# Performance work log

Hardware: AMD Instinct MI355X
Metric: run time of the kernel (lower is better)

The kernel has to match this reference:

```python
import jax, jax.numpy as jnp
import numpy as np

T, N, E = 12, 100000, 3200000
F = H = 64
O, L = 32, 2


def setup_inputs() -> dict:
    key = jax.random.key(0)
    ks = jax.random.split(key, 13)
    sc = 0.08  # keep gate pre-activations in a sane range
    return {
        "x": jax.random.normal(ks[0], (T, N, F), jnp.float32),
        "hidden_states": jax.random.normal(ks[1], (L, N, H), jnp.float32),
        "cell_states": jax.random.normal(ks[2], (L, N, H), jnp.float32),
        "Wx_self": jax.random.normal(ks[3], (L, 4, F, H), jnp.float32) * sc,
        "Wx_neigh": jax.random.normal(ks[4], (L, 4, F, H), jnp.float32) * sc,
        "Wh_self": jax.random.normal(ks[5], (L, 4, H, H), jnp.float32) * sc,
        "Wh_neigh": jax.random.normal(ks[6], (L, 4, H, H), jnp.float32) * sc,
        "w_c": jax.random.normal(ks[7], (L, 3, H), jnp.float32) * sc,  # peephole i,f,o
        "bias": jax.random.normal(ks[8], (L, 4, H), jnp.float32) * sc,  # i,f,c,o
        "Wout": jax.random.normal(ks[9], (H, O), jnp.float32) * sc,
        "bout": jax.random.normal(ks[10], (O,), jnp.float32) * sc,
        "src": jax.random.randint(ks[11], (E,), 0, N, jnp.int32),
        "dst": jax.random.randint(ks[12], (E,), 0, N, jnp.int32),
    }


def reference(x, hidden_states, cell_states, Wx_self, Wx_neigh, Wh_self,
              Wh_neigh, w_c, bias, Wout, bout, src, dst):
    # mean aggregation over incoming edges (DGL copy_u + mean reduce)
    deg = jax.ops.segment_sum(jnp.ones((E,), x.dtype), dst, num_segments=N)
    deg_inv = jnp.where(deg > 0, 1.0 / deg, 0.0)[:, None]  # [N,1]

    def mean_agg(feat):  # [N,D] -> [N,D]
        return jax.ops.segment_sum(feat[src], dst, num_segments=N) * deg_inv

    def gates(feat, agg, Ws, Wn):  # Ws,Wn: [4,D,H] -> [4,N,H]
        return (jnp.einsum('nf,gfh->gnh', feat, Ws)
                + jnp.einsum('nf,gfh->gnh', agg, Wn))

    def step(carry, x_t):
        hs, cs = carry  # [L,N,H] each
        inp = x_t
        new_h, new_c = [], []
        for j in range(L):
            h, c = hs[j], cs[j]
            x_agg = mean_agg(inp)  # reuse_msg_passing: one agg shared by 4 gates
            h_agg = mean_agg(h)
            pre = gates(inp, x_agg, Wx_self[j], Wx_neigh[j]) \
                + gates(h, h_agg, Wh_self[j], Wh_neigh[j])  # [4,N,H]
            i = jax.nn.sigmoid(pre[0] + w_c[j, 0] * c + bias[j, 0])
            f = jax.nn.sigmoid(pre[1] + w_c[j, 1] * c + bias[j, 1])
            c_tilde = jnp.tanh(pre[2] + bias[j, 2])
            nc = f * c + i * c_tilde
            o = jax.nn.sigmoid(pre[3] + w_c[j, 2] * nc + bias[j, 3])
            nh = o * jnp.tanh(nc)
            new_h.append(nh)
            new_c.append(nc)
            inp = nh
        out_t = inp @ Wout + bout  # [N,O]
        return (jnp.stack(new_h), jnp.stack(new_c)), out_t

    (h_f, c_f), outs = jax.lax.scan(step, (hidden_states, cell_states), x)
    return outs, h_f, c_f  # outs: [T,N,O]
```

## Files before the change

kernel.cpp:

```cpp
#include <hip/hip_runtime.h>

#define T_STEPS 12
#define NN 100000
#define EE 3200000
#define HD 64
#define OD 32
#define NBK 391

typedef __attribute__((ext_vector_type(8))) short short8;
typedef __attribute__((ext_vector_type(4))) float f32x4;
typedef __attribute__((ext_vector_type(2))) float f32x2;
typedef unsigned short u16;
typedef unsigned char u8;

__device__ __forceinline__ u16 f2b(float x) {
  union { float f; unsigned u; } v; v.f = x;
  unsigned r = v.u + 0x7FFFu + ((v.u >> 16) & 1u);
  return (u16)(r >> 16);
}
__device__ __forceinline__ u16 f2h(float x) {
  union { _Float16 h; u16 s; } u; u.h = (_Float16)x; return u.s;
}
__device__ __forceinline__ float h2f(u16 s) {
  union { u16 s; _Float16 h; } u; u.s = s; return (float)u.h;
}
__device__ __forceinline__ float sigm(float x) {
  x = fminf(fmaxf(x, -30.f), 30.f);
  return 1.0f / (1.0f + __expf(-x));
}
__device__ __forceinline__ float tanh_f(float x) {
  x = fminf(fmaxf(x, -15.f), 15.f);
  float e = __expf(2.0f * x);
  return (e - 1.0f) / (e + 1.0f);
}

__device__ __forceinline__ uint2 pack8_fp8(const float* f) {
  unsigned lo = 0, hi = 0;
  lo = __builtin_amdgcn_cvt_pk_fp8_f32(f[0], f[1], lo, false);
  lo = __builtin_amdgcn_cvt_pk_fp8_f32(f[2], f[3], lo, true);
  hi = __builtin_amdgcn_cvt_pk_fp8_f32(f[4], f[5], hi, false);
  hi = __builtin_amdgcn_cvt_pk_fp8_f32(f[6], f[7], hi, true);
  return make_uint2(lo, hi);
}
__device__ __forceinline__ u8 f2q(float x) {
  return (u8)(__builtin_amdgcn_cvt_pk_fp8_f32(x, 0.f, 0u, false) & 0xFFu);
}
__device__ __forceinline__ void acc8_fp8(uint2 v, float* a) {
  f32x2 p0 = __builtin_amdgcn_cvt_pk_f32_fp8(v.x, false);
  f32x2 p1 = __builtin_amdgcn_cvt_pk_f32_fp8(v.x, true);
  f32x2 p2 = __builtin_amdgcn_cvt_pk_f32_fp8(v.y, false);
  f32x2 p3 = __builtin_amdgcn_cvt_pk_f32_fp8(v.y, true);
  a[0] += p0[0]; a[1] += p0[1]; a[2] += p1[0]; a[3] += p1[1];
  a[4] += p2[0]; a[5] += p2[1]; a[6] += p3[0]; a[7] += p3[1];
}
__device__ __forceinline__ void dec16_acc2(uint4 q, f32x2* a) {
  a[0] += __builtin_amdgcn_cvt_pk_f32_fp8(q.x, false);
  a[1] += __builtin_amdgcn_cvt_pk_f32_fp8(q.x, true);
  a[2] += __builtin_amdgcn_cvt_pk_f32_fp8(q.y, false);
  a[3] += __builtin_amdgcn_cvt_pk_f32_fp8(q.y, true);
  a[4] += __builtin_amdgcn_cvt_pk_f32_fp8(q.z, false);
  a[5] += __builtin_amdgcn_cvt_pk_f32_fp8(q.z, true);
  a[6] += __builtin_amdgcn_cvt_pk_f32_fp8(q.w, false);
  a[7] += __builtin_amdgcn_cvt_pk_f32_fp8(q.w, true);
}
__device__ __forceinline__ short8 s8_from_fp8(uint2 q) {
  f32x2 p0 = __builtin_amdgcn_cvt_pk_f32_fp8(q.x, false);
  f32x2 p1 = __builtin_amdgcn_cvt_pk_f32_fp8(q.x, true);
  f32x2 p2 = __builtin_amdgcn_cvt_pk_f32_fp8(q.y, false);
  f32x2 p3 = __builtin_amdgcn_cvt_pk_f32_fp8(q.y, true);
  short8 o;
  o[0] = (short)f2b(p0[0]); o[1] = (short)f2b(p0[1]);
  o[2] = (short)f2b(p1[0]); o[3] = (short)f2b(p1[1]);
  o[4] = (short)f2b(p2[0]); o[5] = (short)f2b(p2[1]);
  o[6] = (short)f2b(p3[0]); o[7] = (short)f2b(p3[1]);
  return o;
}
__device__ __forceinline__ short8 s8_from_f32(float4 a, float4 b) {
  short8 o;
  o[0] = (short)f2b(a.x); o[1] = (short)f2b(a.y);
  o[2] = (short)f2b(a.z); o[3] = (short)f2b(a.w);
  o[4] = (short)f2b(b.x); o[5] = (short)f2b(b.y);
  o[6] = (short)f2b(b.z); o[7] = (short)f2b(b.w);
  return o;
}

__global__ __launch_bounds__(256) void k_bhist(const int* __restrict__ dst,
                                               int* __restrict__ bcnt, int E) {
  __shared__ int h[NBK];
  for (int i = threadIdx.x; i < NBK; i += 256) h[i] = 0;
  __syncthreads();
  int base = blockIdx.x * 4096;
#pragma unroll
  for (int i = 0; i < 16; ++i) {
    int e = base + i * 256 + threadIdx.x;
    if (e < E) atomicAdd(&h[dst[e] >> 8], 1);
  }
  __syncthreads();
  for (int i = threadIdx.x; i < NBK; i += 256)
    if (h[i]) atomicAdd(&bcnt[i], h[i]);
}

__global__ __launch_bounds__(512) void k_bscan(const int* __restrict__ bcnt,
                                               int* __restrict__ bbase,
                                               int* __restrict__ bcur) {
  __shared__ int buf[512];
  int tid = threadIdx.x;
  int v = (tid < NBK) ? bcnt[tid] : 0;
  buf[tid] = v;
  __syncthreads();
  for (int off = 1; off < 512; off <<= 1) {
    int t = (tid >= off) ? buf[tid - off] : 0;
    __syncthreads();
    buf[tid] += t;
    __syncthreads();
  }
  if (tid < NBK) {
    int e = buf[tid] - v;
    bbase[tid] = e;
    bcur[tid] = e;
  }
}

__global__ __launch_bounds__(256) void k_bscatter(const int* __restrict__ src,
                                                  const int* __restrict__ dst,
                                                  int* __restrict__ bcur,
                                                  uint2* __restrict__ binned, int E) {
  __shared__ int h[NBK];
  __shared__ int base[NBK];
  __shared__ int cur[NBK];
  for (int i = threadIdx.x; i < NBK; i += 256) { h[i] = 0; cur[i] = 0; }
  __syncthreads();
  int b0 = blockIdx.x * 4096;
  int d[16], s[16];
#pragma unroll
  for (int i = 0; i < 16; ++i) {
    int e = b0 + i * 256 + threadIdx.x;
    if (e < E) {
      d[i] = dst[e];
      s[i] = src[e];
      atomicAdd(&h[d[i] >> 8], 1);
    } else d[i] = -1;
  }
  __syncthreads();
  for (int i = threadIdx.x; i < NBK; i += 256)
    if (h[i]) base[i] = atomicAdd(&bcur[i], h[i]);
  __syncthreads();
#pragma unroll
  for (int i = 0; i < 16; ++i) {
    if (d[i] >= 0) {
      int bk = d[i] >> 8;
      int r = atomicAdd(&cur[bk], 1);
      binned[base[bk] + r] = make_uint2((unsigned)s[i], (unsigned)d[i]);
    }
  }
}

__global__ __launch_bounds__(256) void k_bsort(const uint2* __restrict__ binned,
                                               const int* __restrict__ bbase,
                                               const int* __restrict__ bcnt,
                                               int* __restrict__ csr,
                                               int* __restrict__ row_ptr,
                                               float* __restrict__ deg_inv, int n) {
  __shared__ int cnt[256];
  __shared__ int buf[256];
  __shared__ int cur[256];
  int b = blockIdx.x, tid = threadIdx.x;
  int ebase = bbase[b];
  int ecnt = bcnt[b];
  cnt[tid] = 0;
  __syncthreads();
  for (int i = tid; i < ecnt; i += 256)
    atomicAdd(&cnt[binned[ebase + i].y & 255], 1);
  __syncthreads();
  int v = cnt[tid];
  buf[tid] = v;
  __syncthreads();
  for (int off = 1; off < 256; off <<= 1) {
    int t = (tid >= off) ? buf[tid - off] : 0;
    __syncthreads();
    buf[tid] += t;
    __syncthreads();
  }
  int excl = buf[tid] - v;
  int node = b * 256 + tid;
  if (node < n) {
    row_ptr[node] = ebase + excl;
    deg_inv[node] = v ? (1.0f / (float)v) : 0.0f;
  }
  if (b == NBK - 1 && tid == 0) row_ptr[n] = ebase + ecnt;
  cur[tid] = excl;
  __syncthreads();
  for (int i = tid; i < ecnt; i += 256) {
    uint2 pr = binned[ebase + i];
    int pos = atomicAdd(&cur[pr.y & 255], 1);
    csr[ebase + pos] = (int)pr.x;
  }
}

__global__ __launch_bounds__(256) void k_prep(const float* __restrict__ Wxs,
                                              const float* __restrict__ Wxn,
                                              const float* __restrict__ Whs,
                                              const float* __restrict__ Whn,
                                              u16* __restrict__ bprep) {
  int idx = blockIdx.x * 256 + threadIdx.x;
  int l = idx >> 16;
  int kb = (idx >> 13) & 7;
  int fi = (idx >> 9) & 15;
  int ln = (idx >> 3) & 63;
  int j = idx & 7;
  int fc = kb * 32 + ((ln >> 4) << 3) + j;
  int g = fi & 3;
  int kk = ((fi >> 2) << 4) + (ln & 15);
  int t = fc >> 6, f = fc & 63;
  const float* tabs[4] = {Wxs, Wxn, Whs, Whn};
  bprep[idx] = f2b(tabs[t][((size_t)(l * 4 + g) * 64 + f) * 64 + kk]);
}

__global__ __launch_bounds__(256) void k_prepw(const float* __restrict__ Wout,
                                               u16* __restrict__ wp) {
  int idx = blockIdx.x * 256 + threadIdx.x;
  int kb = idx >> 10;
  int fi = (idx >> 9) & 1;
  int ln = (idx >> 3) & 63;
  int j = idx & 7;
  int k = kb * 32 + ((ln >> 4) << 3) + j;
  int o = fi * 16 + (ln & 15);
  wp[idx] = f2b(Wout[k * 32 + o]);
}

__global__ __launch_bounds__(256) void k_convxall(const float* __restrict__ x,
                                                  u8* __restrict__ XQ) {
  int tid = blockIdx.x * 256 + threadIdx.x;
  int j = tid & 7;
  int tn = tid >> 3;
  int n = tn % NN;
  int t = tn / NN;
  const float* rp = x + (size_t)tn * 64 + j * 8;
  float4 v0 = *reinterpret_cast<const float4*>(rp);
  float4 v1 = *reinterpret_cast<const float4*>(rp + 4);
  float f[8] = {v0.x, v0.y, v0.z, v0.w, v1.x, v1.y, v1.z, v1.w};
  *reinterpret_cast<uint2*>(XQ + (size_t)n * 768 + t * 64 + j * 8) = pack8_fp8(f);
}

__global__ __launch_bounds__(256) void k_inith(const float* __restrict__ h0,
                                               const float* __restrict__ c0,
                                               u16* __restrict__ H0bf,
                                               u16* __restrict__ L1bf,
                                               u8* __restrict__ HQ,
                                               u16* __restrict__ C16) {
  int idx = blockIdx.x * 256 + threadIdx.x;
  int n = idx >> 3, j = idx & 7;
#pragma unroll
  for (int L = 0; L < 2; ++L) {
    const float* rp = h0 + (size_t)L * NN * 64 + (size_t)n * 64 + j * 8;
    float4 v0 = *reinterpret_cast<const float4*>(rp);
    float4 v1 = *reinterpret_cast<const float4*>(rp + 4);
    float f[8] = {v0.x, v0.y, v0.z, v0.w, v1.x, v1.y, v1.z, v1.w};
    short8 o;
#pragma unroll
    for (int i = 0; i < 8; ++i) o[i] = (short)f2b(f[i]);
    if (L == 0)
      *reinterpret_cast<short8*>(H0bf + (size_t)n * 64 + j * 8) = o;
    else
      *reinterpret_cast<short8*>(L1bf + (size_t)n * 64 + j * 8) = o;
    *reinterpret_cast<uint2*>(HQ + (size_t)n * 128 + L * 64 + j * 8) = pack8_fp8(f);
    const float* cp = c0 + (size_t)L * NN * 64 + (size_t)n * 64 + j * 8;
    float4 c0v = *reinterpret_cast<const float4*>(cp);
    float4 c1v = *reinterpret_cast<const float4*>(cp + 4);
    float cf[8] = {c0v.x, c0v.y, c0v.z, c0v.w, c1v.x, c1v.y, c1v.z, c1v.w};
    short8 oc;
#pragma unroll
    for (int i = 0; i < 8; ++i) oc[i] = (short)f2h(cf[i]);
    *reinterpret_cast<short8*>(C16 + (size_t)L * NN * 64 + (size_t)n * 64 + j * 8) = oc;
  }
}

__global__ __launch_bounds__(256) void k_aggx(const u8* __restrict__ XQ,
                                              const int* __restrict__ row_ptr,
                                              const int* __restrict__ csr,
                                              const float* __restrict__ deg_inv,
                                              u8* __restrict__ AGGXq) {
  int node = blockIdx.x * 4 + (threadIdx.x >> 6);
  int p = blockIdx.y;
  int lane = threadIdx.x & 63;
  int g = lane >> 4, m = lane & 15;
  int start = row_ptr[node], end = row_ptr[node + 1];
  const size_t poff = (size_t)p * 256 + m * 16;
  f32x2 a[8];
#pragma unroll
  for (int i = 0; i < 8; ++i) a[i] = (f32x2){0.f, 0.f};
  int e = start + g;
  for (; e + 12 < end; e += 16) {
    int s0 = csr[e], s1 = csr[e + 4], s2 = csr[e + 8], s3 = csr[e + 12];
    uint4 q0 = *reinterpret_cast<const uint4*>(XQ + (size_t)s0 * 768 + poff);
    uint4 q1 = *reinterpret_cast<const uint4*>(XQ + (size_t)s1 * 768 + poff);
    uint4 q2 = *reinterpret_cast<const uint4*>(XQ + (size_t)s2 * 768 + poff);
    uint4 q3 = *reinterpret_cast<const uint4*>(XQ + (size_t)s3 * 768 + poff);
    dec16_acc2(q0, a); dec16_acc2(q1, a); dec16_acc2(q2, a); dec16_acc2(q3, a);
  }
  if (e + 4 < end) {
    int s0 = csr[e], s1 = csr[e + 4];
    uint4 q0 = *reinterpret_cast<const uint4*>(XQ + (size_t)s0 * 768 + poff);
    uint4 q1 = *reinterpret_cast<const uint4*>(XQ + (size_t)s1 * 768 + poff);
    dec16_acc2(q0, a); dec16_acc2(q1, a);
    e += 8;
  }
  if (e < end) {
    int s0 = csr[e];
    uint4 q0 = *reinterpret_cast<const uint4*>(XQ + (size_t)s0 * 768 + poff);
    dec16_acc2(q0, a);
  }
#pragma unroll
  for (int off = 16; off < 64; off <<= 1)
#pragma unroll
    for (int i = 0; i < 8; ++i) {
      a[i][0] += __shfl_xor(a[i][0], off);
      a[i][1] += __shfl_xor(a[i][1], off);
    }
  if (g == 0) {
    float sc = deg_inv[node];
    float f[16];
#pragma unroll
    for (int i = 0; i < 8; ++i) {
      f[i * 2] = a[i][0] * sc;
      f[i * 2 + 1] = a[i][1] * sc;
    }
    uint4 o;
    unsigned w;
    w = 0; w = __builtin_amdgcn_cvt_pk_fp8_f32(f[0], f[1], w, false);
    w = __builtin_amdgcn_cvt_pk_fp8_f32(f[2], f[3], w, true); o.x = w;
    w = 0; w = __builtin_amdgcn_cvt_pk_fp8_f32(f[4], f[5], w, false);
    w = __builtin_amdgcn_cvt_pk_fp8_f32(f[6], f[7], w, true); o.y = w;
    w = 0; w = __builtin_amdgcn_cvt_pk_fp8_f32(f[8], f[9], w, false);
    w = __builtin_amdgcn_cvt_pk_fp8_f32(f[10], f[11], w, true); o.z = w;
    w = 0; w = __builtin_amdgcn_cvt_pk_fp8_f32(f[12], f[13], w, false);
    w = __builtin_amdgcn_cvt_pk_fp8_f32(f[14], f[15], w, true); o.w = w;
    int t = p * 4 + (m >> 2);
    *reinterpret_cast<uint4*>(AGGXq + ((size_t)t * NN + node) * 64 + (m & 3) * 16) = o;
  }
}

__global__ __launch_bounds__(256) void k_agg_pair(const u8* __restrict__ Q,
                                                  const int* __restrict__ row_ptr,
                                                  const int* __restrict__ csr,
                                                  const float* __restrict__ deg_inv,
                                                  u16* __restrict__ out0,
                                                  u16* __restrict__ out1) {
  int node = blockIdx.x * 4 + (threadIdx.x >> 6);
  int lane = threadIdx.x & 63;
  int g = lane >> 4, m = lane & 15;
  int start = row_ptr[node], end = row_ptr[node + 1];
  float a[8] = {0, 0, 0, 0, 0, 0, 0, 0};
  int e = start + g;
  for (; e + 12 < end; e += 16) {
    int s0 = csr[e], s1 = csr[e + 4], s2 = csr[e + 8], s3 = csr[e + 12];
    uint2 v0 = *reinterpret_cast<const uint2*>(Q + (size_t)s0 * 128 + m * 8);
    uint2 v1 = *reinterpret_cast<const uint2*>(Q + (size_t)s1 * 128 + m * 8);
    uint2 v2 = *reinterpret_cast<const uint2*>(Q + (size_t)s2 * 128 + m * 8);
    uint2 v3 = *reinterpret_cast<const uint2*>(Q + (size_t)s3 * 128 + m * 8);
    acc8_fp8(v0, a); acc8_fp8(v1, a); acc8_fp8(v2, a); acc8_fp8(v3, a);
  }
  if (e + 4 < end) {
    int s0 = csr[e], s1 = csr[e + 4];
    uint2 v0 = *reinterpret_cast<const uint2*>(Q + (size_t)s0 * 128 + m * 8);
    uint2 v1 = *reinterpret_cast<const uint2*>(Q + (size_t)s1 * 128 + m * 8);
    acc8_fp8(v0, a); acc8_fp8(v1, a);
    e += 8;
  }
  if (e < end) {
    int s0 = csr[e];
    uint2 v0 = *reinterpret_cast<const uint2*>(Q + (size_t)s0 * 128 + m * 8);
    acc8_fp8(v0, a);
  }
#pragma unroll
  for (int off = 16; off < 64; off <<= 1) {
#pragma unroll
    for (int i = 0; i < 8; ++i) a[i] += __shfl_xor(a[i], off);
  }
  if (g == 0) {
    float sc = deg_inv[node];
    short8 o;
#pragma unroll
    for (int i = 0; i < 8; ++i) o[i] = (short)f2b(a[i] * sc);
    if (m < 8)
      *reinterpret_cast<short8*>(out0 + (size_t)node * 64 + m * 8) = o;
    else
      *reinterpret_cast<short8*>(out1 + (size_t)node * 64 + (m - 8) * 8) = o;
  }
}

__global__ __launch_bounds__(256, 2) void k_gates0(
    const float* __restrict__ xin, const u8* __restrict__ aggxq,
    u16* __restrict__ h0bf, const u16* __restrict__ aggh0,
    u8* __restrict__ hq, u16* __restrict__ c16,
    float* __restrict__ hf32, float* __restrict__ cf32,
    const u16* __restrict__ bprepl,
    const float* __restrict__ wcl, const float* __restrict__ biasl,
    int n_nodes, int wf) {
  const int tid = threadIdx.x;
  const int lane = tid & 63;
  const int w = tid >> 6;
  const int nb = blockIdx.x * 64;
  const int cl = lane & 15;
  const int kg = lane >> 4;

  short8 breg[8][4];
#pragma unroll
  for (int kb = 0; kb < 8; ++kb)
#pragma unroll
    for (int fl = 0; fl < 4; ++fl)
      breg[kb][fl] = *reinterpret_cast<const short8*>(
          bprepl + (kb << 13) + (((w << 2) + fl) << 9) + (lane << 3));

  int gnc[4];
#pragma unroll
  for (int rg = 0; rg < 4; ++rg) {
    int g = nb + rg * 16 + cl;
    gnc[rg] = (g < n_nodes) ? g : (n_nodes - 1);
  }

  f32x4 acc[4][4];
  f32x4 z4 = {0.f, 0.f, 0.f, 0.f};
#pragma unroll
  for (int a = 0; a < 4; ++a)
#pragma unroll
    for (int b = 0; b < 4; ++b) acc[a][b] = z4;

  const int koff = kg << 3;
#pragma unroll
  for (int kb = 0; kb < 8; ++kb) {
    const int idx = ((kb & 1) << 5) + koff;
#pragma unroll
    for (int rg = 0; rg < 4; ++rg) {
      short8 a;
      if (kb < 2) {
        const float* rp = xin + (size_t)gnc[rg] * 64 + idx;
        a = s8_from_f32(*reinterpret_cast<const float4*>(rp),
                        *reinterpret_cast<const float4*>(rp + 4));
      } else if (kb < 4) {
        a = s8_from_fp8(*reinterpret_cast<const uint2*>(aggxq + (size_t)gnc[rg] * 64 + idx));
      } else if (kb < 6) {
        a = *reinterpret_cast<const short8*>(h0bf + (size_t)gnc[rg] * 64 + idx);
      } else {
        a = *reinterpret_cast<const short8*>(aggh0 + (size_t)gnc[rg] * 64 + idx);
      }
      acc[rg][0] = __builtin_amdgcn_mfma_f32_16x16x32_bf16(a, breg[kb][0], acc[rg][0], 0, 0, 0);
      acc[rg][1] = __builtin_amdgcn_mfma_f32_16x16x32_bf16(a, breg[kb][1], acc[rg][1], 0, 0, 0);
      acc[rg][2] = __builtin_amdgcn_mfma_f32_16x16x32_bf16(a, breg[kb][2], acc[rg][2], 0, 0, 0);
      acc[rg][3] = __builtin_amdgcn_mfma_f32_16x16x32_bf16(a, breg[kb][3], acc[rg][3], 0, 0, 0);
    }
  }
  __syncthreads();

  const int k = (w << 4) + cl;
  const float wci = wcl[k], wcf = wcl[64 + k], wco = wcl[128 + k];
  const float bi = biasl[k], bfg = biasl[64 + k], bc = biasl[128 + k], bo = biasl[192 + k];
#pragma unroll
  for (int rg = 0; rg < 4; ++rg) {
#pragma unroll
    for (int r = 0; r < 4; ++r) {
      int n = nb + rg * 16 + kg * 4 + r;
      if (n < n_nodes) {
        size_t off = (size_t)n * 64 + k;
        float c_old = h2f(c16[off]);
        float ig = sigm(acc[rg][0][r] + wci * c_old + bi);
        float fg = sigm(acc[rg][1][r] + wcf * c_old + bfg);
        float ct = tanh_f(acc[rg][2][r] + bc);
        float nc = fg * c_old + ig * ct;
        float og = sigm(acc[rg][3][r] + wco * nc + bo);
        float nh = og * tanh_f(nc);
        c16[off] = f2h(nc);
        h0bf[off] = f2b(nh);
        hq[(size_t)n * 128 + k] = f2q(nh);
        if (wf) { hf32[off] = nh; cf32[off] = nc; }
      }
    }
  }
}

__global__ __launch_bounds__(256, 2) void k_gates1(
    const u16* __restrict__ h0bf, const u16* __restrict__ aggh0,
    const u16* __restrict__ aggh1,
    u16* __restrict__ l1bf, u8* __restrict__ hq, u16* __restrict__ c16,
    float* __restrict__ hf32, float* __restrict__ cf32,
    const u16* __restrict__ bprepl,
    const float* __restrict__ wcl, const float* __restrict__ biasl,
    const u16* __restrict__ wproj, const float* __restrict__ boutp,
    float* __restrict__ outp, int n_nodes, int wf) {
  __shared__ u16 Hsm[64 * 64];
  const int tid = threadIdx.x;
  const int lane = tid & 63;
  const int w = tid >> 6;
  const int nb = blockIdx.x * 64;
  const int cl = lane & 15;
  const int kg = lane >> 4;

  short8 breg[8][4];
#pragma unroll
  for (int kb = 0; kb < 8; ++kb)
#pragma unroll
    for (int fl = 0; fl < 4; ++fl)
      breg[kb][fl] = *reinterpret_cast<const short8*>(
          bprepl + (kb << 13) + (((w << 2) + fl) << 9) + (lane << 3));

  int gnc[4];
#pragma unroll
  for (int rg = 0; rg < 4; ++rg) {
    int g = nb + rg * 16 + cl;
    gnc[rg] = (g < n_nodes) ? g : (n_nodes - 1);
  }

  f32x4 acc[4][4];
  f32x4 z4 = {0.f, 0.f, 0.f, 0.f};
#pragma unroll
  for (int a = 0; a < 4; ++a)
#pragma unroll
    for (int b = 0; b < 4; ++b) acc[a][b] = z4;

  const int koff = kg << 3;
#pragma unroll
  for (int kb = 0; kb < 8; ++kb) {
    const int idx = ((kb & 1) << 5) + koff;
#pragma unroll
    for (int rg = 0; rg < 4; ++rg) {
      short8 a;
      if (kb < 2) {
        a = *reinterpret_cast<const short8*>(h0bf + (size_t)gnc[rg] * 64 + idx);
      } else if (kb < 4) {
        a = *reinterpret_cast<const short8*>(aggh0 + (size_t)gnc[rg] * 64 + idx);
      } else if (kb < 6) {
        a = *reinterpret_cast<const short8*>(l1bf + (size_t)gnc[rg] * 64 + idx);
      } else {
        a = *reinterpret_cast<const short8*>(aggh1 + (size_t)gnc[rg] * 64 + idx);
      }
      acc[rg][0] = __builtin_amdgcn_mfma_f32_16x16x32_bf16(a, breg[kb][0], acc[rg][0], 0, 0, 0);
      acc[rg][1] = __builtin_amdgcn_mfma_f32_16x16x32_bf16(a, breg[kb][1], acc[rg][1], 0, 0, 0);
      acc[rg][2] = __builtin_amdgcn_mfma_f32_16x16x32_bf16(a, breg[kb][2], acc[rg][2], 0, 0, 0);
      acc[rg][3] = __builtin_amdgcn_mfma_f32_16x16x32_bf16(a, breg[kb][3], acc[rg][3], 0, 0, 0);
    }
  }
  __syncthreads();

  const int k = (w << 4) + cl;
  const float wci = wcl[k], wcf = wcl[64 + k], wco = wcl[128 + k];
  const float bi = biasl[k], bfg = biasl[64 + k], bc = biasl[128 + k], bo = biasl[192 + k];
#pragma unroll
  for (int rg = 0; rg < 4; ++rg) {
#pragma unroll
    for (int r = 0; r < 4; ++r) {
      int n = nb + rg * 16 + kg * 4 + r;
      if (n < n_nodes) {
        size_t off = (size_t)n * 64 + k;
        float c_old = h2f(c16[off]);
        float ig = sigm(acc[rg][0][r] + wci * c_old + bi);
        float fg = sigm(acc[rg][1][r] + wcf * c_old + bfg);
        float ct = tanh_f(acc[rg][2][r] + bc);
        float nc = fg * c_old + ig * ct;
        float og = sigm(acc[rg][3][r] + wco * nc + bo);
        float nh = og * tanh_f(nc);
        c16[off] = f2h(nc);
        u16 hb = f2b(nh);
        l1bf[off] = hb;
        hq[(size_t)n * 128 + 64 + k] = f2q(nh);
        Hsm[(rg * 16 + kg * 4 + r) * 64 + k] = hb;
        if (wf) { hf32[off] = nh; cf32[off] = nc; }
      }
    }
  }

  __syncthreads();
  short8 bw[2][2];
#pragma unroll
  for (int kb = 0; kb < 2; ++kb)
#pragma unroll
    for (int fi = 0; fi < 2; ++fi)
      bw[kb][fi] = *reinterpret_cast<const short8*>(wproj + (((kb * 2 + fi) * 64 + lane) << 3));
  short8 a0 = *reinterpret_cast<const short8*>(&Hsm[(w * 16 + cl) * 64 + kg * 8]);
  short8 a1 = *reinterpret_cast<const short8*>(&Hsm[(w * 16 + cl) * 64 + 32 + kg * 8]);
  f32x4 p0 = z4, p1 = z4;
  p0 = __builtin_amdgcn_mfma_f32_16x16x32_bf16(a0, bw[0][0], p0, 0, 0, 0);
  p0 = __builtin_amdgcn_mfma_f32_16x16x32_bf16(a1, bw[1][0], p0, 0, 0, 0);
  p1 = __builtin_amdgcn_mfma_f32_16x16x32_bf16(a0, bw[0][1], p1, 0, 0, 0);
  p1 = __builtin_amdgcn_mfma_f32_16x16x32_bf16(a1, bw[1][1], p1, 0, 0, 0);
  const float bo0 = boutp[cl], bo1 = boutp[16 + cl];
#pragma unroll
  for (int r = 0; r < 4; ++r) {
    int n = nb + w * 16 + kg * 4 + r;
    if (n < n_nodes) {
      outp[(size_t)n * OD + cl] = p0[r] + bo0;
      outp[(size_t)n * OD + 16 + cl] = p1[r] + bo1;
    }
  }
}

extern "C" void kernel_launch(void* const* d_in, const int* in_sizes, int n_in,
                              void* d_out, int out_size, void* d_ws, size_t ws_size,
                              hipStream_t stream) {
  const float* x = (const float*)d_in[0];
  const float* h0 = (const float*)d_in[1];
  const float* c0 = (const float*)d_in[2];
  const float* Wxs = (const float*)d_in[3];
  const float* Wxn = (const float*)d_in[4];
  const float* Whs = (const float*)d_in[5];
  const float* Whn = (const float*)d_in[6];
  const float* wc = (const float*)d_in[7];
  const float* bias = (const float*)d_in[8];
  const float* Wout = (const float*)d_in[9];
  const float* bout = (const float*)d_in[10];
  const int* src = (const int*)d_in[11];
  const int* dst = (const int*)d_in[12];

  float* out = (float*)d_out;
  float* outs = out;
  float* hstate = out + (size_t)T_STEPS * NN * OD;
  float* cstate = hstate + (size_t)2 * NN * HD;

  char* p = (char*)d_ws;
  auto alloc = [&](size_t bytes) {
    char* r = p;
    p += (bytes + 255) & ~(size_t)255;
    return r;
  };
  int* csr = (int*)alloc((size_t)EE * 4);
  u8* XQ = (u8*)alloc((size_t)NN * 768);
  uint2* binned = (uint2*)XQ;
  u8* AGGXq = (u8*)alloc((size_t)T_STEPS * NN * 64);
  int* row_ptr = (int*)alloc((size_t)(NN + 1) * 4);
  int* bcnt = (int*)alloc(NBK * 4);
  int* bbase = (int*)alloc(NBK * 4);
  int* bcur = (int*)alloc(NBK * 4);
  float* deg_inv = (float*)alloc((size_t)NN * 4);
  u16* H0bf = (u16*)alloc((size_t)NN * 64 * 2);
  u16* L1bf = (u16*)alloc((size_t)NN * 64 * 2);
  u8* HQ = (u8*)alloc((size_t)NN * 128);
  u16* AGGH0 = (u16*)alloc((size_t)NN * 64 * 2);
  u16* AGGH1 = (u16*)alloc((size_t)NN * 64 * 2);
  u16* C16 = (u16*)alloc((size_t)2 * NN * 64 * 2);
  u16* bprep = (u16*)alloc((size_t)2 * 65536 * 2);
  u16* wprep = (u16*)alloc((size_t)2048 * 2);

  const int nchunk = (EE + 4095) / 4096;

  hipMemsetAsync(bcnt, 0, (size_t)NBK * 4, stream);
  k_bhist<<<nchunk, 256, 0, stream>>>(dst, bcnt, EE);
  k_bscan<<<1, 512, 0, stream>>>(bcnt, bbase, bcur);
  k_bscatter<<<nchunk, 256, 0, stream>>>(src, dst, bcur, binned, EE);
  k_bsort<<<NBK, 256, 0, stream>>>(binned, bbase, bcnt, csr, row_ptr, deg_inv, NN);
  k_prep<<<512, 256, 0, stream>>>(Wxs, Wxn, Whs, Whn, bprep);
  k_prepw<<<8, 256, 0, stream>>>(Wout, wprep);
  k_convxall<<<(T_STEPS * NN * 8 + 255) / 256, 256, 0, stream>>>(x, XQ);
  k_inith<<<NN * 8 / 256, 256, 0, stream>>>(h0, c0, H0bf, L1bf, HQ, C16);
  {
    dim3 g((NN + 3) / 4, 3);
    k_aggx<<<g, 256, 0, stream>>>(XQ, row_ptr, csr, deg_inv, AGGXq);
  }
  k_agg_pair<<<(NN + 3) / 4, 256, 0, stream>>>(HQ, row_ptr, csr, deg_inv, AGGH0, AGGH1);

  for (int t = 0; t < T_STEPS; ++t) {
    int wf = (t == T_STEPS - 1) ? 1 : 0;
    k_gates0<<<(NN + 63) / 64, 256, 0, stream>>>(
        x + (size_t)t * NN * HD, AGGXq + (size_t)t * NN * 64,
        H0bf, AGGH0, HQ, C16, hstate, cstate, bprep, wc, bias, NN, wf);
    k_agg_pair<<<(NN + 3) / 4, 256, 0, stream>>>(HQ, row_ptr, csr, deg_inv, AGGH0, AGGH1);
    k_gates1<<<(NN + 63) / 64, 256, 0, stream>>>(
        H0bf, AGGH0, AGGH1, L1bf, HQ, C16 + (size_t)NN * 64,
        hstate + (size_t)NN * HD, cstate + (size_t)NN * HD,
        bprep + 65536, wc + 192, bias + 256,
        wprep, bout, outs + (size_t)t * NN * OD, NN, wf);
  }
}
```

Measured before the change: 2.887 ms.

## Fuse per-step neighbor aggregation into layer-1 gates kernel with LDS staging

Removes the separate per-step pair aggregation kernel. The layer-1 gate kernel now gathers the fp8 neighbor features for both layers itself, stores them in swizzled shared memory and feeds them straight into the MFMA loop. It also writes AGGH0 out for the next step's layer-0 kernel. The interleaved fp8 hidden table is split into separate layer-0 and layer-1 tables, and layer 1 is double-buffered so in-place updates do not race with neighbor reads from other blocks. This saves a launch and the bf16 aggregate round-trip through global memory. In exchange the gates kernel uses more shared memory and becomes a latency-bound gather, which may lower occupancy.

Result: slower. 3.231 ms (+11.9%).

```diff
diff --git a/kernel.cpp b/kernel.cpp
--- a/kernel.cpp
+++ b/kernel.cpp
@@ -44,14 +44,6 @@
 }
 __device__ __forceinline__ u8 f2q(float x) {
   return (u8)(__builtin_amdgcn_cvt_pk_fp8_f32(x, 0.f, 0u, false) & 0xFFu);
-}
-__device__ __forceinline__ void acc8_fp8(uint2 v, float* a) {
-  f32x2 p0 = __builtin_amdgcn_cvt_pk_f32_fp8(v.x, false);
-  f32x2 p1 = __builtin_amdgcn_cvt_pk_f32_fp8(v.x, true);
-  f32x2 p2 = __builtin_amdgcn_cvt_pk_f32_fp8(v.y, false);
-  f32x2 p3 = __builtin_amdgcn_cvt_pk_f32_fp8(v.y, true);
-  a[0] += p0[0]; a[1] += p0[1]; a[2] += p1[0]; a[3] += p1[1];
-  a[4] += p2[0]; a[5] += p2[1]; a[6] += p3[0]; a[7] += p3[1];
 }
 __device__ __forceinline__ void dec16_acc2(uint4 q, f32x2* a) {
   a[0] += __builtin_amdgcn_cvt_pk_f32_fp8(q.x, false);
@@ -246,7 +238,8 @@
                                                const float* __restrict__ c0,
                                                u16* __restrict__ H0bf,
                                                u16* __restrict__ L1bf,
-                                               u8* __restrict__ HQ,
+                                               u8* __restrict__ HQ0,
+                                               u8* __restrict__ HQ1,
                                                u16* __restrict__ C16) {
   int idx = blockIdx.x * 256 + threadIdx.x;
   int n = idx >> 3, j = idx & 7;
@@ -259,11 +252,13 @@
     short8 o;
 #pragma unroll
     for (int i = 0; i < 8; ++i) o[i] = (short)f2b(f[i]);
-    if (L == 0)
+    if (L == 0) {
       *reinterpret_cast<short8*>(H0bf + (size_t)n * 64 + j * 8) = o;
-    else
+      *reinterpret_cast<uint2*>(HQ0 + (size_t)n * 64 + j * 8) = pack8_fp8(f);
+    } else {
       *reinterpret_cast<short8*>(L1bf + (size_t)n * 64 + j * 8) = o;
-    *reinterpret_cast<uint2*>(HQ + (size_t)n * 128 + L * 64 + j * 8) = pack8_fp8(f);
+      *reinterpret_cast<uint2*>(HQ1 + (size_t)n * 64 + j * 8) = pack8_fp8(f);
+    }
     const float* cp = c0 + (size_t)L * NN * 64 + (size_t)n * 64 + j * 8;
     float4 c0v = *reinterpret_cast<const float4*>(cp);
     float4 c1v = *reinterpret_cast<const float4*>(cp + 4);
@@ -340,59 +335,53 @@
   }
 }
 
-__global__ __launch_bounds__(256) void k_agg_pair(const u8* __restrict__ Q,
-                                                  const int* __restrict__ row_ptr,
-                                                  const int* __restrict__ csr,
-                                                  const float* __restrict__ deg_inv,
-                                                  u16* __restrict__ out0,
-                                                  u16* __restrict__ out1) {
-  int node = blockIdx.x * 4 + (threadIdx.x >> 6);
+__global__ __launch_bounds__(256) void k_agg0(const u8* __restrict__ HQ0,
+                                              const int* __restrict__ row_ptr,
+                                              const int* __restrict__ csr,
+                                              const float* __restrict__ deg_inv,
+                                              u16* __restrict__ aggh0, int n_nodes) {
   int lane = threadIdx.x & 63;
-  int g = lane >> 4, m = lane & 15;
-  int start = row_ptr[node], end = row_ptr[node + 1];
-  float a[8] = {0, 0, 0, 0, 0, 0, 0, 0};
-  int e = start + g;
-  for (; e + 12 < end; e += 16) {
-    int s0 = csr[e], s1 = csr[e + 4], s2 = csr[e + 8], s3 = csr[e + 12];
-    uint2 v0 = *reinterpret_cast<const uint2*>(Q + (size_t)s0 * 128 + m * 8);
-    uint2 v1 = *reinterpret_cast<const uint2*>(Q + (size_t)s1 * 128 + m * 8);
-    uint2 v2 = *reinterpret_cast<const uint2*>(Q + (size_t)s2 * 128 + m * 8);
-    uint2 v3 = *reinterpret_cast<const uint2*>(Q + (size_t)s3 * 128 + m * 8);
-    acc8_fp8(v0, a); acc8_fp8(v1, a); acc8_fp8(v2, a); acc8_fp8(v3, a);
-  }
-  if (e + 4 < end) {
-    int s0 = csr[e], s1 = csr[e + 4];
-    uint2 v0 = *reinterpret_cast<const uint2*>(Q + (size_t)s0 * 128 + m * 8);
-    uint2 v1 = *reinterpret_cast<const uint2*>(Q + (size_t)s1 * 128 + m * 8);
-    acc8_fp8(v0, a); acc8_fp8(v1, a);
-    e += 8;
-  }
-  if (e < end) {
-    int s0 = csr[e];
-    uint2 v0 = *reinterpret_cast<const uint2*>(Q + (size_t)s0 * 128 + m * 8);
-    acc8_fp8(v0, a);
-  }
-#pragma unroll
-  for (int off = 16; off < 64; off <<= 1) {
-#pragma unroll
-    for (int i = 0; i < 8; ++i) a[i] += __shfl_xor(a[i], off);
-  }
-  if (g == 0) {
+  int w = threadIdx.x >> 6;
+  int ng = lane >> 2, m = lane & 3;
+  int node = blockIdx.x * 64 + w * 16 + ng;
+  int nodec = (node < n_nodes) ? node : (n_nodes - 1);
+  int start = row_ptr[nodec], end = row_ptr[nodec + 1];
+  const int coff = m * 16;
+  f32x2 a[8];
+#pragma unroll
+  for (int i = 0; i < 8; ++i) a[i] = (f32x2){0.f, 0.f};
+  int e = start;
+  for (; e + 3 < end; e += 4) {
+    int s0 = csr[e], s1 = csr[e + 1], s2 = csr[e + 2], s3 = csr[e + 3];
+    uint4 q0 = *reinterpret_cast<const uint4*>(HQ0 + (size_t)s0 * 64 + coff);
+    uint4 q1 = *reinterpret_cast<const uint4*>(HQ0 + (size_t)s1 * 64 + coff);
+    uint4 q2 = *reinterpret_cast<const uint4*>(HQ0 + (size_t)s2 * 64 + coff);
+    uint4 q3 = *reinterpret_cast<const uint4*>(HQ0 + (size_t)s3 * 64 + coff);
+    dec16_acc2(q0, a); dec16_acc2(q1, a); dec16_acc2(q2, a); dec16_acc2(q3, a);
+  }
+  for (; e < end; ++e) {
+    uint4 q0 = *reinterpret_cast<const uint4*>(HQ0 + (size_t)csr[e] * 64 + coff);
+    dec16_acc2(q0, a);
+  }
+  if (node < n_nodes) {
     float sc = deg_inv[node];
-    short8 o;
-#pragma unroll
-    for (int i = 0; i < 8; ++i) o[i] = (short)f2b(a[i] * sc);
-    if (m < 8)
-      *reinterpret_cast<short8*>(out0 + (size_t)node * 64 + m * 8) = o;
-    else
-      *reinterpret_cast<short8*>(out1 + (size_t)node * 64 + (m - 8) * 8) = o;
+    short8 o0, o1;
+#pragma unroll
+    for (int i = 0; i < 4; ++i) {
+      o0[i * 2] = (short)f2b(a[i][0] * sc);
+      o0[i * 2 + 1] = (short)f2b(a[i][1] * sc);
+      o1[i * 2] = (short)f2b(a[4 + i][0] * sc);
+      o1[i * 2 + 1] = (short)f2b(a[4 + i][1] * sc);
+    }
+    *reinterpret_cast<short8*>(aggh0 + (size_t)node * 64 + m * 16) = o0;
+    *reinterpret_cast<short8*>(aggh0 + (size_t)node * 64 + m * 16 + 8) = o1;
   }
 }
 
 __global__ __launch_bounds__(256, 2) void k_gates0(
     const float* __restrict__ xin, const u8* __restrict__ aggxq,
     u16* __restrict__ h0bf, const u16* __restrict__ aggh0,
-    u8* __restrict__ hq, u16* __restrict__ c16,
+    u8* __restrict__ hq0, u16* __restrict__ c16,
     float* __restrict__ hf32, float* __restrict__ cf32,
     const u16* __restrict__ bprepl,
     const float* __restrict__ wcl, const float* __restrict__ biasl,
@@ -471,30 +460,84 @@
         float nh = og * tanh_f(nc);
         c16[off] = f2h(nc);
         h0bf[off] = f2b(nh);
-        hq[(size_t)n * 128 + k] = f2q(nh);
+        hq0[off] = f2q(nh);
         if (wf) { hf32[off] = nh; cf32[off] = nc; }
       }
     }
   }
 }
 
-__global__ __launch_bounds__(256, 2) void k_gates1(
-    const u16* __restrict__ h0bf, const u16* __restrict__ aggh0,
-    const u16* __restrict__ aggh1,
-    u16* __restrict__ l1bf, u8* __restrict__ hq, u16* __restrict__ c16,
+__global__ __launch_bounds__(256, 2) void k_pg1(
+    const u8* __restrict__ HQ0, const u8* __restrict__ HQ1r,
+    u8* __restrict__ HQ1w,
+    const int* __restrict__ row_ptr, const int* __restrict__ csr,
+    const float* __restrict__ deg_inv,
+    u16* __restrict__ aggh0,
+    const u16* __restrict__ h0bf, u16* __restrict__ l1bf, u16* __restrict__ c16,
     float* __restrict__ hf32, float* __restrict__ cf32,
     const u16* __restrict__ bprepl,
     const float* __restrict__ wcl, const float* __restrict__ biasl,
     const u16* __restrict__ wproj, const float* __restrict__ boutp,
     float* __restrict__ outp, int n_nodes, int wf) {
+  __shared__ __align__(16) u8 A0sm[64 * 128];
+  __shared__ __align__(16) u8 A1sm[64 * 128];
   __shared__ u16 Hsm[64 * 64];
   const int tid = threadIdx.x;
   const int lane = tid & 63;
   const int w = tid >> 6;
   const int nb = blockIdx.x * 64;
+
+  {
+    const int grp = lane >> 3;
+    const int m = lane & 7;
+    const u8* tab = (m < 4) ? HQ0 : HQ1r;
+    const int coff = (m & 3) * 16;
+#pragma unroll
+    for (int round = 0; round < 2; ++round) {
+      int nl = w * 16 + round * 8 + grp;
+      int node = nb + nl;
+      int nodec = (node < n_nodes) ? node : (n_nodes - 1);
+      int start = row_ptr[nodec], end = row_ptr[nodec + 1];
+      f32x2 a[8];
+#pragma unroll
+      for (int i = 0; i < 8; ++i) a[i] = (f32x2){0.f, 0.f};
+      int e = start;
+      for (; e + 3 < end; e += 4) {
+        int s0 = csr[e], s1 = csr[e + 1], s2 = csr[e + 2], s3 = csr[e + 3];
+        uint4 q0 = *reinterpret_cast<const uint4*>(tab + (size_t)s0 * 64 + coff);
+        uint4 q1 = *reinterpret_cast<const uint4*>(tab + (size_t)s1 * 64 + coff);
+        uint4 q2 = *reinterpret_cast<const uint4*>(tab + (size_t)s2 * 64 + coff);
+        uint4 q3 = *reinterpret_cast<const uint4*>(tab + (size_t)s3 * 64 + coff);
+        dec16_acc2(q0, a); dec16_acc2(q1, a); dec16_acc2(q2, a); dec16_acc2(q3, a);
+      }
+      for (; e < end; ++e) {
+        uint4 q0 = *reinterpret_cast<const uint4*>(tab + (size_t)csr[e] * 64 + coff);
+        dec16_acc2(q0, a);
+      }
+      float sc = deg_inv[nodec];
+      short8 o0, o1;
+#pragma unroll
+      for (int i = 0; i < 4; ++i) {
+        o0[i * 2] = (short)f2b(a[i][0] * sc);
+        o0[i * 2 + 1] = (short)f2b(a[i][1] * sc);
+        o1[i * 2] = (short)f2b(a[4 + i][0] * sc);
+        o1[i * 2 + 1] = (short)f2b(a[4 + i][1] * sc);
+      }
+      u8* dstsm = (m < 4) ? A0sm : A1sm;
+      int cb0 = ((m & 3) * 32) ^ ((nl & 7) << 4);
+      int cb1 = ((m & 3) * 32 + 16) ^ ((nl & 7) << 4);
+      *reinterpret_cast<short8*>(dstsm + nl * 128 + cb0) = o0;
+      *reinterpret_cast<short8*>(dstsm + nl * 128 + cb1) = o1;
+      if (m < 4 && node < n_nodes) {
+        *reinterpret_cast<short8*>(aggh0 + (size_t)node * 64 + (m & 3) * 16) = o0;
+        *reinterpret_cast<short8*>(aggh0 + (size_t)node * 64 + (m & 3) * 16 + 8) = o1;
+      }
+    }
+  }
+  __syncthreads();
+
   const int cl = lane & 15;
   const int kg = lane >> 4;
-
   short8 breg[8][4];
 #pragma unroll
   for (int kb = 0; kb < 8; ++kb)
@@ -524,14 +567,16 @@
 #pragma unroll
     for (int rg = 0; rg < 4; ++rg) {
       short8 a;
+      int nlr = rg * 16 + cl;
+      int cbyte = (((kb & 1) << 6) + (koff << 1)) ^ ((nlr & 7) << 4);
       if (kb < 2) {
         a = *reinterpret_cast<const short8*>(h0bf + (size_t)gnc[rg] * 64 + idx);
       } else if (kb < 4) {
-        a = *reinterpret_cast<const short8*>(aggh0 + (size_t)gnc[rg] * 64 + idx);
+        a = *reinterpret_cast<const short8*>(A0sm + nlr * 128 + cbyte);
       } else if (kb < 6) {
         a = *reinterpret_cast<const short8*>(l1bf + (size_t)gnc[rg] * 64 + idx);
       } else {
-        a = *reinterpret_cast<const short8*>(aggh1 + (size_t)gnc[rg] * 64 + idx);
+        a = *reinterpret_cast<const short8*>(A1sm + nlr * 128 + cbyte);
       }
       acc[rg][0] = __builtin_amdgcn_mfma_f32_16x16x32_bf16(a, breg[kb][0], acc[rg][0], 0, 0, 0);
       acc[rg][1] = __builtin_amdgcn_mfma_f32_16x16x32_bf16(a, breg[kb][1], acc[rg][1], 0, 0, 0);
@@ -561,7 +606,7 @@
         c16[off] = f2h(nc);
         u16 hb = f2b(nh);
         l1bf[off] = hb;
-        hq[(size_t)n * 128 + 64 + k] = f2q(nh);
+        HQ1w[off] = f2q(nh);
         Hsm[(rg * 16 + kg * 4 + r) * 64 + k] = hb;
         if (wf) { hf32[off] = nh; cf32[off] = nc; }
       }
@@ -632,9 +677,9 @@
   float* deg_inv = (float*)alloc((size_t)NN * 4);
   u16* H0bf = (u16*)alloc((size_t)NN * 64 * 2);
   u16* L1bf = (u16*)alloc((size_t)NN * 64 * 2);
-  u8* HQ = (u8*)alloc((size_t)NN * 128);
+  u8* HQ0 = (u8*)alloc((size_t)NN * 64);
+  u8* HQ1 = (u8*)alloc((size_t)2 * NN * 64);
   u16* AGGH0 = (u16*)alloc((size_t)NN * 64 * 2);
-  u16* AGGH1 = (u16*)alloc((size_t)NN * 64 * 2);
   u16* C16 = (u16*)alloc((size_t)2 * NN * 64 * 2);
   u16* bprep = (u16*)alloc((size_t)2 * 65536 * 2);
   u16* wprep = (u16*)alloc((size_t)2048 * 2);
@@ -649,21 +694,22 @@
   k_prep<<<512, 256, 0, stream>>>(Wxs, Wxn, Whs, Whn, bprep);
   k_prepw<<<8, 256, 0, stream>>>(Wout, wprep);
   k_convxall<<<(T_STEPS * NN * 8 + 255) / 256, 256, 0, stream>>>(x, XQ);
-  k_inith<<<NN * 8 / 256, 256, 0, stream>>>(h0, c0, H0bf, L1bf, HQ, C16);
+  k_inith<<<NN * 8 / 256, 256, 0, stream>>>(h0, c0, H0bf, L1bf, HQ0, HQ1, C16);
   {
     dim3 g((NN + 3) / 4, 3);
     k_aggx<<<g, 256, 0, stream>>>(XQ, row_ptr, csr, deg_inv, AGGXq);
   }
-  k_agg_pair<<<(NN + 3) / 4, 256, 0, stream>>>(HQ, row_ptr, csr, deg_inv, AGGH0, AGGH1);
+  k_agg0<<<(NN + 63) / 64, 256, 0, stream>>>(HQ0, row_ptr, csr, deg_inv, AGGH0, NN);
 
   for (int t = 0; t < T_STEPS; ++t) {
     int wf = (t == T_STEPS - 1) ? 1 : 0;
     k_gates0<<<(NN + 63) / 64, 256, 0, stream>>>(
         x + (size_t)t * NN * HD, AGGXq + (size_t)t * NN * 64,
-        H0bf, AGGH0, HQ, C16, hstate, cstate, bprep, wc, bias, NN, wf);
-    k_agg_pair<<<(NN + 3) / 4, 256, 0, stream>>>(HQ, row_ptr, csr, deg_inv, AGGH0, AGGH1);
-    k_gates1<<<(NN + 63) / 64, 256, 0, stream>>>(
-        H0bf, AGGH0, AGGH1, L1bf, HQ, C16 + (size_t)NN * 64,
+        H0bf, AGGH0, HQ0, C16, hstate, cstate, bprep, wc, bias, NN, wf);
+    k_pg1<<<(NN + 63) / 64, 256, 0, stream>>>(
+        HQ0, HQ1 + (size_t)(t & 1) * NN * 64, HQ1 + (size_t)((t + 1) & 1) * NN * 64,
+        row_ptr, csr, deg_inv, AGGH0,
+        H0bf, L1bf, C16 + (size_t)NN * 64,
         hstate + (size_t)NN * HD, cstate + (size_t)NN * HD,
         bprep + 65536, wc + 192, bias + 256,
         wprep, bout, outs + (size_t)t * NN * OD, NN, wf);
```
